# Kernel optimization log

Measured on AMD Instinct MI355X. Metric: run time of the kernel, lower is better.

The kernel has to match this reference:

```python
import jax, jax.numpy as jnp
import numpy as np

H = 2048        # hidden_size
E = 64          # num_experts
TOPK = 4        # top_k_experts
EPS = 1e-6      # rms_norm_eps
SW = 1024       # sliding_window
NEG = jnp.finfo(jnp.float32).min


def setup_inputs() -> dict:
    key = jax.random.key(0)
    k1, k2, k3, k4, k5 = jax.random.split(key, 5)
    B, S = 2, 4096
    x = jax.random.normal(k1, (B, S, H), jnp.float32)
    # 1-based document ids packed contiguously; 0 = padding
    packed_seq_ids = jnp.sort(jax.random.randint(k2, (B, S), 0, 5), axis=-1)
    # 0 = text, 1/2 = vision tokens
    mm_token_type_ids = jax.random.randint(k3, (B, S), 0, 3)
    scale = jax.random.uniform(k4, (H,), jnp.float32, 0.5, 1.5)
    proj_w = jax.random.normal(k5, (E, H), jnp.float32) * 0.02
    return dict(x=x, packed_seq_ids=packed_seq_ids,
                mm_token_type_ids=mm_token_type_ids, scale=scale, proj_w=proj_w)


def _vision_group_ids(mm):
    # per-image-block ids for vision tokens, -1 for text/padding
    is_v = (mm == 1) | (mm == 2)
    is_prev = jnp.concatenate([jnp.zeros_like(is_v[:, :1]), is_v[:, :-1]], axis=-1)
    starts = is_v & ~is_prev
    gid = jnp.cumsum(starts.astype(jnp.int32), axis=1) - 1
    return jnp.where(is_v, gid, -1)


def _build_masks(packed, mm, sliding_window):
    B, S = packed.shape
    pos = jnp.arange(S)
    causal = pos[None, :, None] >= pos[None, None, :]          # [1,S,S] kv<=q
    valid_q = packed[:, :, None] > 0
    valid_kv = packed[:, None, :] > 0
    same_doc = (packed[:, :, None] == packed[:, None, :]) & valid_q & valid_kv
    full = same_doc & causal                                   # [B,S,S]
    sliding = full & ((pos[None, :, None] - pos[None, None, :]) < sliding_window)
    gid = _vision_group_ids(mm)
    same_vg = (gid[:, :, None] == gid[:, None, :]) & (gid[:, :, None] >= 0)
    sliding = (sliding | same_vg) & same_doc
    # additive format, [B,1,S,S]
    full_add = jnp.where(full[:, None], jnp.float32(0.0), NEG)
    sliding_add = jnp.where(sliding[:, None], jnp.float32(0.0), NEG)
    return full_add, sliding_add


def _gate(x, scale, proj_w):
    # Gemma4Gate: RMSNorm(no scale) -> H**-0.5 -> learnable scale -> linear
    #             -> softmax -> top-k -> renormalize
    xf = x.reshape(-1, H)                                      # [N,H]
    xn = xf * jax.lax.rsqrt(jnp.mean(xf * xf, axis=-1, keepdims=True) + EPS)
    xn = xn * (H ** -0.5) * scale
    logits = jnp.einsum('nh,eh->ne', xn, proj_w)               # [N,E]
    probs = jax.nn.softmax(logits, axis=-1)
    weights, indices = jax.lax.top_k(probs, TOPK)              # [N,K]
    weights = weights / jnp.maximum(jnp.sum(weights, axis=-1, keepdims=True), 1e-20)
    return weights, indices


def reference(x, packed_seq_ids, mm_token_type_ids, scale, proj_w):
    full_mask, sliding_mask = _build_masks(packed_seq_ids, mm_token_type_ids, SW)
    weights, indices = _gate(x, scale, proj_w)
    return full_mask, sliding_mask, weights, indices
```

## Files before the change

kernel.cpp:

```cpp
#include <hip/hip_runtime.h>
#include <math.h>

#define S 4096
#define HH 2048
#define NE 64
#define SW 1024
#define MASKED 0xFBFFu

typedef unsigned short u16;
typedef unsigned int u32;

__device__ __align__(16) int g_gid[2 * S];
__device__ __align__(16) float g_pw2[NE * HH];

__device__ __forceinline__ float h2f(u32 lo16) {
    union { u16 u; _Float16 h; } v; v.u = (u16)lo16; return (float)v.h;
}
__device__ __forceinline__ u16 f2h(float f) {
    union { u16 u; _Float16 h; } v; v.h = (_Float16)f; return v.u;
}
__device__ __forceinline__ void u4_to_f8(uint4 v, float* o) {
    o[0] = h2f(v.x & 0xFFFFu); o[1] = h2f(v.x >> 16);
    o[2] = h2f(v.y & 0xFFFFu); o[3] = h2f(v.y >> 16);
    o[4] = h2f(v.z & 0xFFFFu); o[5] = h2f(v.z >> 16);
    o[6] = h2f(v.w & 0xFFFFu); o[7] = h2f(v.w >> 16);
}

__global__ __launch_bounds__(256) void pre_kernel(const int* __restrict__ mm,
                                                  const u16* __restrict__ proj_w) {
    const int blk = blockIdx.x;
    const int t = threadIdx.x;
    if (blk < 2) {
        __shared__ int ts[256];
        const int* m = mm + blk * S;
        const int base_pos = t * 16;
        int vals[16];
#pragma unroll
        for (int i = 0; i < 16; i++) vals[i] = m[base_pos + i];
        bool prevv = false;
        if (base_pos > 0) {
            int pv = m[base_pos - 1];
            prevv = (pv == 1) || (pv == 2);
        }
        int cnt = 0;
        {
            bool pv = prevv;
#pragma unroll
            for (int i = 0; i < 16; i++) {
                bool is = (vals[i] == 1) || (vals[i] == 2);
                cnt += (is && !pv) ? 1 : 0;
                pv = is;
            }
        }
        ts[t] = cnt;
        __syncthreads();
        for (int off = 1; off < 256; off <<= 1) {
            int add = (t >= off) ? ts[t - off] : 0;
            __syncthreads();
            ts[t] += add;
            __syncthreads();
        }
        int base = ts[t] - cnt;
        {
            bool pv = prevv;
            int run = base;
#pragma unroll
            for (int i = 0; i < 16; i++) {
                bool is = (vals[i] == 1) || (vals[i] == 2);
                run += (is && !pv) ? 1 : 0;
                g_gid[blk * S + base_pos + i] = is ? (run - 1) : -1;
                pv = is;
            }
        }
    } else {
        int idx = (blk - 2) * 256 + t;
        int e = idx >> 11;
        int h = idx & 2047;
        g_pw2[(h >> 2) * 256 + e * 4 + (h & 3)] = h2f((u32)proj_w[idx]);
    }
}

__global__ __launch_bounds__(256) void mask_kernel(const int* __restrict__ packed,
                                                   u16* __restrict__ full_out,
                                                   u16* __restrict__ slid_out) {
    const int tid = blockIdx.x * 256 + threadIdx.x;
    const int kc = tid & 511;
    const int q = (tid >> 9) & 4095;
    const int b = tid >> 21;
    const int k0 = kc * 8;

    const int pq = packed[b * S + q];
    const int gq = g_gid[b * S + q];
    const int4 pk0 = *(const int4*)(packed + b * S + k0);
    const int4 pk1 = *(const int4*)(packed + b * S + k0 + 4);
    const int4 gk0 = *(const int4*)(g_gid + b * S + k0);
    const int4 gk1 = *(const int4*)(g_gid + b * S + k0 + 4);

    int pkj[8] = {pk0.x, pk0.y, pk0.z, pk0.w, pk1.x, pk1.y, pk1.z, pk1.w};
    int gkj[8] = {gk0.x, gk0.y, gk0.z, gk0.w, gk1.x, gk1.y, gk1.z, gk1.w};
    u32 fm[8], sm[8];
#pragma unroll
    for (int j = 0; j < 8; j++) {
        int k = k0 + j;
        bool sd = (pq > 0) && (pkj[j] == pq);
        bool fl = sd && (q >= k);
        bool sl = ((fl && ((q - k) < SW)) || ((gkj[j] == gq) && (gq >= 0))) && sd;
        fm[j] = fl ? 0u : MASKED;
        sm[j] = sl ? 0u : MASKED;
    }
    uint4 f4, s4;
    f4.x = fm[0] | (fm[1] << 16); f4.y = fm[2] | (fm[3] << 16);
    f4.z = fm[4] | (fm[5] << 16); f4.w = fm[6] | (fm[7] << 16);
    s4.x = sm[0] | (sm[1] << 16); s4.y = sm[2] | (sm[3] << 16);
    s4.z = sm[4] | (sm[5] << 16); s4.w = sm[6] | (sm[7] << 16);

    size_t off = (size_t)b * ((size_t)S * S) + (size_t)q * S + k0;
    *(uint4*)(full_out + off) = f4;
    *(uint4*)(slid_out + off) = s4;
}

__global__ __launch_bounds__(256) void gate_kernel(const u16* __restrict__ x,
                                                   const u16* __restrict__ scale,
                                                   u16* __restrict__ w_out,
                                                   u16* __restrict__ i_out) {
    __shared__ float factor[16];
    __shared__ float xs[16][132];
    __shared__ float part[4][16][65];

    const int t = threadIdx.x;
    const int w = t >> 6;
    const int l = t & 63;
    const int tok0 = blockIdx.x * 16;

    for (int tt = w; tt < 16; tt += 4) {
        const uint4* xp = (const uint4*)(x + (size_t)(tok0 + tt) * HH);
        float ss = 0.0f;
#pragma unroll
        for (int j = 0; j < 4; j++) {
            float o[8];
            u4_to_f8(xp[l + 64 * j], o);
#pragma unroll
            for (int i = 0; i < 8; i++) ss += o[i] * o[i];
        }
        for (int off = 32; off >= 1; off >>= 1) ss += __shfl_xor(ss, off);
        if (l == 0)
            factor[tt] = rsqrtf(ss * (1.0f / 2048.0f) + 1e-6f) * 0.022097086912079608f;
    }
    __syncthreads();

    float acc[16];
#pragma unroll
    for (int i = 0; i < 16; i++) acc[i] = 0.0f;

    const int stok = t >> 4;
    const int sh = (t & 15) * 8;

    for (int ch = 0; ch < 16; ch++) {
        {
            uint4 xv = *(const uint4*)(x + (size_t)(tok0 + stok) * HH + ch * 128 + sh);
            uint4 sv = *(const uint4*)(scale + ch * 128 + sh);
            float xo[8], so[8];
            u4_to_f8(xv, xo);
            u4_to_f8(sv, so);
            float fac = factor[stok];
            float4 a, b;
            a.x = xo[0] * fac * so[0]; a.y = xo[1] * fac * so[1];
            a.z = xo[2] * fac * so[2]; a.w = xo[3] * fac * so[3];
            b.x = xo[4] * fac * so[4]; b.y = xo[5] * fac * so[5];
            b.z = xo[6] * fac * so[6]; b.w = xo[7] * fac * so[7];
            *(float4*)&xs[stok][sh] = a;
            *(float4*)&xs[stok][sh + 4] = b;
        }
        __syncthreads();

        const float4* pwp = ((const float4*)g_pw2) + (size_t)(ch * 32 + w * 8) * 64 + l;
#pragma unroll
        for (int i = 0; i < 8; i++) {
            float4 p4 = pwp[(size_t)i * 64];
#pragma unroll
            for (int tok = 0; tok < 16; tok++) {
                float4 xv = *(const float4*)&xs[tok][w * 32 + i * 4];
                acc[tok] += p4.x * xv.x + p4.y * xv.y + p4.z * xv.z + p4.w * xv.w;
            }
        }
        __syncthreads();
    }

#pragma unroll
    for (int tok = 0; tok < 16; tok++) part[w][tok][l] = acc[tok];
    __syncthreads();

    {
        int tok = t >> 4;
        int eg = t & 15;
        float lg[4];
#pragma unroll
        for (int j = 0; j < 4; j++) {
            int e = eg * 4 + j;
            lg[j] = part[0][tok][e] + part[1][tok][e] + part[2][tok][e] + part[3][tok][e];
        }
        *(float4*)&xs[tok][eg * 4] = make_float4(lg[0], lg[1], lg[2], lg[3]);
    }
    __syncthreads();

    if (t < 16) {
        unsigned long long used = 0ull;
        float bv[4];
        int bi[4];
#pragma unroll
        for (int p = 0; p < 4; p++) {
            float best = -INFINITY;
            int besti = 0;
            for (int e = 0; e < NE; e++) {
                if (used & (1ull << e)) continue;
                float v = xs[t][e];
                if (v > best) { best = v; besti = e; }
            }
            used |= 1ull << besti;
            bv[p] = best;
            bi[p] = besti;
        }
        float ww[4];
        float ssum = 0.0f;
#pragma unroll
        for (int p = 0; p < 4; p++) { ww[p] = expf(bv[p] - bv[0]); ssum += ww[p]; }
        int n = tok0 + t;
#pragma unroll
        for (int p = 0; p < 4; p++) {
            w_out[n * 4 + p] = f2h(ww[p] / ssum);
            i_out[n * 4 + p] = f2h((float)bi[p]);
        }
    }
}

extern "C" void kernel_launch(void* const* d_in, const int* in_sizes, int n_in,
                              void* d_out, int out_size, void* d_ws, size_t ws_size,
                              hipStream_t stream) {
    const u16* x = (const u16*)d_in[0];
    const int* packed = (const int*)d_in[1];
    const int* mm = (const int*)d_in[2];
    const u16* scale = (const u16*)d_in[3];
    const u16* proj_w = (const u16*)d_in[4];

    u16* out = (u16*)d_out;
    u16* full_out = out;
    u16* slid_out = out + 33554432;
    u16* w_out = out + 67108864;
    u16* i_out = out + 67141632;

    pre_kernel<<<514, 256, 0, stream>>>(mm, proj_w);
    mask_kernel<<<16384, 256, 0, stream>>>(packed, full_out, slid_out);
    gate_kernel<<<512, 256, 0, stream>>>(x, scale, w_out, i_out);
    (void)in_sizes; (void)n_in; (void)out_size; (void)d_ws; (void)ws_size;
}
```

Before: 369.9 us.

## Fuse mask and gate kernels into one launch with register-tiled gate GEMV

Merges the mask kernel and gate kernel into a single launch, with the first 512 blocks doing the gate and the rest writing masks, so the compute-bound gate overlaps with the bandwidth-bound mask writes. The gate inner loop is retiled to a 4-token by 4-expert register block per lane, which improves reuse of projection weights and x loads. The next chunk's x and scale are prefetched into registers. The tradeoff is that the mask blocks now carry the gate kernel's shared memory allocation, which may lower their occupancy.

```diff
diff --git a/kernel.cpp b/kernel.cpp
--- a/kernel.cpp
+++ b/kernel.cpp
@@ -80,54 +80,56 @@
     }
 }
 
-__global__ __launch_bounds__(256) void mask_kernel(const int* __restrict__ packed,
-                                                   u16* __restrict__ full_out,
-                                                   u16* __restrict__ slid_out) {
-    const int tid = blockIdx.x * 256 + threadIdx.x;
-    const int kc = tid & 511;
-    const int q = (tid >> 9) & 4095;
-    const int b = tid >> 21;
-    const int k0 = kc * 8;
-
-    const int pq = packed[b * S + q];
-    const int gq = g_gid[b * S + q];
-    const int4 pk0 = *(const int4*)(packed + b * S + k0);
-    const int4 pk1 = *(const int4*)(packed + b * S + k0 + 4);
-    const int4 gk0 = *(const int4*)(g_gid + b * S + k0);
-    const int4 gk1 = *(const int4*)(g_gid + b * S + k0 + 4);
-
-    int pkj[8] = {pk0.x, pk0.y, pk0.z, pk0.w, pk1.x, pk1.y, pk1.z, pk1.w};
-    int gkj[8] = {gk0.x, gk0.y, gk0.z, gk0.w, gk1.x, gk1.y, gk1.z, gk1.w};
-    u32 fm[8], sm[8];
-#pragma unroll
-    for (int j = 0; j < 8; j++) {
-        int k = k0 + j;
-        bool sd = (pq > 0) && (pkj[j] == pq);
-        bool fl = sd && (q >= k);
-        bool sl = ((fl && ((q - k) < SW)) || ((gkj[j] == gq) && (gq >= 0))) && sd;
-        fm[j] = fl ? 0u : MASKED;
-        sm[j] = sl ? 0u : MASKED;
-    }
-    uint4 f4, s4;
-    f4.x = fm[0] | (fm[1] << 16); f4.y = fm[2] | (fm[3] << 16);
-    f4.z = fm[4] | (fm[5] << 16); f4.w = fm[6] | (fm[7] << 16);
-    s4.x = sm[0] | (sm[1] << 16); s4.y = sm[2] | (sm[3] << 16);
-    s4.z = sm[4] | (sm[5] << 16); s4.w = sm[6] | (sm[7] << 16);
-
-    size_t off = (size_t)b * ((size_t)S * S) + (size_t)q * S + k0;
-    *(uint4*)(full_out + off) = f4;
-    *(uint4*)(slid_out + off) = s4;
-}
-
-__global__ __launch_bounds__(256) void gate_kernel(const u16* __restrict__ x,
-                                                   const u16* __restrict__ scale,
-                                                   u16* __restrict__ w_out,
-                                                   u16* __restrict__ i_out) {
+__global__ __launch_bounds__(256) void fused_kernel(
+    const u16* __restrict__ x, const u16* __restrict__ scale,
+    const int* __restrict__ packed,
+    u16* __restrict__ full_out, u16* __restrict__ slid_out,
+    u16* __restrict__ w_out, u16* __restrict__ i_out) {
+
     __shared__ float factor[16];
     __shared__ float xs[16][132];
     __shared__ float part[4][16][65];
 
     const int t = threadIdx.x;
+
+    if (blockIdx.x >= 512) {
+        const int tid = (blockIdx.x - 512) * 256 + t;
+        const int kc = tid & 511;
+        const int q = (tid >> 9) & 4095;
+        const int b = tid >> 21;
+        const int k0 = kc * 8;
+
+        const int pq = packed[b * S + q];
+        const int gq = g_gid[b * S + q];
+        const int4 pk0 = *(const int4*)(packed + b * S + k0);
+        const int4 pk1 = *(const int4*)(packed + b * S + k0 + 4);
+        const int4 gk0 = *(const int4*)(g_gid + b * S + k0);
+        const int4 gk1 = *(const int4*)(g_gid + b * S + k0 + 4);
+
+        int pkj[8] = {pk0.x, pk0.y, pk0.z, pk0.w, pk1.x, pk1.y, pk1.z, pk1.w};
+        int gkj[8] = {gk0.x, gk0.y, gk0.z, gk0.w, gk1.x, gk1.y, gk1.z, gk1.w};
+        u32 fm[8], sm[8];
+#pragma unroll
+        for (int j = 0; j < 8; j++) {
+            int k = k0 + j;
+            bool sd = (pq > 0) && (pkj[j] == pq);
+            bool fl = sd && (q >= k);
+            bool sl = ((fl && ((q - k) < SW)) || ((gkj[j] == gq) && (gq >= 0))) && sd;
+            fm[j] = fl ? 0u : MASKED;
+            sm[j] = sl ? 0u : MASKED;
+        }
+        uint4 f4, s4;
+        f4.x = fm[0] | (fm[1] << 16); f4.y = fm[2] | (fm[3] << 16);
+        f4.z = fm[4] | (fm[5] << 16); f4.w = fm[6] | (fm[7] << 16);
+        s4.x = sm[0] | (sm[1] << 16); s4.y = sm[2] | (sm[3] << 16);
+        s4.z = sm[4] | (sm[5] << 16); s4.w = sm[6] | (sm[7] << 16);
+
+        size_t off = (size_t)b * ((size_t)S * S) + (size_t)q * S + k0;
+        *(uint4*)(full_out + off) = f4;
+        *(uint4*)(slid_out + off) = s4;
+        return;
+    }
+
     const int w = t >> 6;
     const int l = t & 63;
     const int tok0 = blockIdx.x * 16;
@@ -148,20 +150,27 @@
     }
     __syncthreads();
 
-    float acc[16];
-#pragma unroll
-    for (int i = 0; i < 16; i++) acc[i] = 0.0f;
+    const int g = l & 15;
+    const int ts = l >> 4;
+    float acc[4][4];
+#pragma unroll
+    for (int a = 0; a < 4; a++)
+#pragma unroll
+        for (int bb = 0; bb < 4; bb++) acc[a][bb] = 0.0f;
 
     const int stok = t >> 4;
     const int sh = (t & 15) * 8;
+    const u16* xrow = x + (size_t)(tok0 + stok) * HH + sh;
+
+    uint4 xv_p = *(const uint4*)(xrow);
+    uint4 sv_p = *(const uint4*)(scale + sh);
 
     for (int ch = 0; ch < 16; ch++) {
+        __syncthreads();
         {
-            uint4 xv = *(const uint4*)(x + (size_t)(tok0 + stok) * HH + ch * 128 + sh);
-            uint4 sv = *(const uint4*)(scale + ch * 128 + sh);
             float xo[8], so[8];
-            u4_to_f8(xv, xo);
-            u4_to_f8(sv, so);
+            u4_to_f8(xv_p, xo);
+            u4_to_f8(sv_p, so);
             float fac = factor[stok];
             float4 a, b;
             a.x = xo[0] * fac * so[0]; a.y = xo[1] * fac * so[1];
@@ -172,22 +181,34 @@
             *(float4*)&xs[stok][sh + 4] = b;
         }
         __syncthreads();
-
-        const float4* pwp = ((const float4*)g_pw2) + (size_t)(ch * 32 + w * 8) * 64 + l;
+        if (ch < 15) {
+            xv_p = *(const uint4*)(xrow + (ch + 1) * 128);
+            sv_p = *(const uint4*)(scale + (ch + 1) * 128 + sh);
+        }
+
+        const float* pwb = g_pw2 + (size_t)(ch * 32 + w * 8) * 256 + g * 16;
 #pragma unroll
         for (int i = 0; i < 8; i++) {
-            float4 p4 = pwp[(size_t)i * 64];
-#pragma unroll
-            for (int tok = 0; tok < 16; tok++) {
-                float4 xv = *(const float4*)&xs[tok][w * 32 + i * 4];
-                acc[tok] += p4.x * xv.x + p4.y * xv.y + p4.z * xv.z + p4.w * xv.w;
-            }
-        }
-        __syncthreads();
-    }
-
-#pragma unroll
-    for (int tok = 0; tok < 16; tok++) part[w][tok][l] = acc[tok];
+            float4 p[4];
+#pragma unroll
+            for (int ej = 0; ej < 4; ej++)
+                p[ej] = *(const float4*)(pwb + (size_t)i * 256 + ej * 4);
+#pragma unroll
+            for (int tk = 0; tk < 4; tk++) {
+                float4 xv = *(const float4*)&xs[4 * ts + tk][w * 32 + i * 4];
+#pragma unroll
+                for (int ej = 0; ej < 4; ej++)
+                    acc[tk][ej] += p[ej].x * xv.x + p[ej].y * xv.y +
+                                   p[ej].z * xv.z + p[ej].w * xv.w;
+            }
+        }
+    }
+
+#pragma unroll
+    for (int tk = 0; tk < 4; tk++)
+#pragma unroll
+        for (int ej = 0; ej < 4; ej++)
+            part[w][4 * ts + tk][4 * g + ej] = acc[tk][ej];
     __syncthreads();
 
     {
@@ -249,7 +270,7 @@
     u16* i_out = out + 67141632;
 
     pre_kernel<<<514, 256, 0, stream>>>(mm, proj_w);
-    mask_kernel<<<16384, 256, 0, stream>>>(packed, full_out, slid_out);
-    gate_kernel<<<512, 256, 0, stream>>>(x, scale, w_out, i_out);
+    fused_kernel<<<512 + 16384, 256, 0, stream>>>(x, scale, packed,
+                                                  full_out, slid_out, w_out, i_out);
     (void)in_sizes; (void)n_in; (void)out_size; (void)d_ws; (void)ws_size;
 }
```

After: 361.7 us. -2.2%, faster.
